# Kernel tuning notes

Measured on AMD Instinct MI355X. Metric: run time of the kernel, lower is better.

Reference implementation:

```python
import jax, jax.numpy as jnp
import numpy as np

HEADS = 4
OUT_CH = 32
NEG_SLOPE = 0.2  # PyG GATConv default leaky_relu slope


def setup_inputs() -> dict:
    key = jax.random.key(0)
    ks = jax.random.split(key, 8)
    N, E, C_IN = 500000, 1500000, 128
    x = jax.random.normal(ks[0], (N, C_IN), dtype=jnp.float32)
    edge_index = jax.random.randint(ks[1], (2, E), 0, N, dtype=jnp.int64)
    # GATConv params (lin weight, attention vectors, bias)
    W = jax.random.normal(ks[2], (C_IN, HEADS * OUT_CH), dtype=jnp.float32) * (1.0 / np.sqrt(C_IN))
    att_src = jax.random.normal(ks[3], (HEADS, OUT_CH), dtype=jnp.float32) * 0.1
    att_dst = jax.random.normal(ks[4], (HEADS, OUT_CH), dtype=jnp.float32) * 0.1
    bias = jnp.zeros((HEADS * OUT_CH,), dtype=jnp.float32)
    # fc head
    fc_w = jax.random.normal(ks[5], (HEADS * OUT_CH, 1), dtype=jnp.float32) * (1.0 / np.sqrt(HEADS * OUT_CH))
    fc_b = jnp.zeros((1,), dtype=jnp.float32)
    return {"x": x, "edge_index": edge_index, "W": W, "att_src": att_src,
            "att_dst": att_dst, "bias": bias, "fc_w": fc_w, "fc_b": fc_b}


def reference(x, edge_index, W, att_src, att_dst, bias, fc_w, fc_b):
    N = x.shape[0]
    # PyG GATConv adds self-loops by default
    loops = jnp.arange(N, dtype=edge_index.dtype)
    src = jnp.concatenate([edge_index[0], loops])  # [Etot]
    dst = jnp.concatenate([edge_index[1], loops])  # [Etot]

    h = (x @ W).reshape(N, HEADS, OUT_CH)                # [N,H,C]
    a_src = jnp.einsum('nhc,hc->nh', h, att_src)          # [N,H]
    a_dst = jnp.einsum('nhc,hc->nh', h, att_dst)          # [N,H]

    e = a_src[src] + a_dst[dst]                           # [Etot,H]
    e = jax.nn.leaky_relu(e, NEG_SLOPE)
    # segment softmax over incoming edges of each dst node
    e_max = jax.ops.segment_max(e, dst, num_segments=N)   # [N,H]
    e_exp = jnp.exp(e - e_max[dst])
    e_sum = jax.ops.segment_sum(e_exp, dst, num_segments=N)
    alpha = e_exp / e_sum[dst]                            # [Etot,H]

    msg = h[src] * alpha[:, :, None]                      # [Etot,H,C]
    out = jax.ops.segment_sum(msg, dst, num_segments=N)   # [N,H,C]
    out = out.reshape(N, HEADS * OUT_CH) + bias

    out = jax.nn.relu(out)
    logits = out @ fc_w + fc_b                            # [N,1]
    return jax.nn.sigmoid(logits)
```

## Files before the change

kernel.cpp:

```cpp
#include <hip/hip_runtime.h>

typedef __attribute__((ext_vector_type(8))) short bf16x8;
typedef __attribute__((ext_vector_type(4))) float f32x4;

__device__ __forceinline__ unsigned short f2bf(float f){
  unsigned int u = __builtin_bit_cast(unsigned int, f);
  u += 0x7fffu + ((u >> 16) & 1u);
  return (unsigned short)(u >> 16);
}
__device__ __forceinline__ float bf_lo(unsigned int v){
  return __builtin_bit_cast(float, v << 16);
}
__device__ __forceinline__ float bf_hi(unsigned int v){
  return __builtin_bit_cast(float, v & 0xffff0000u);
}
__device__ __forceinline__ float lrelu(float x){ return x > 0.f ? x : 0.2f * x; }

#define GLOAD_LDS16(g, l) \
  __builtin_amdgcn_global_load_lds((const __attribute__((address_space(1))) unsigned int*)(g), \
                                   (__attribute__((address_space(3))) unsigned int*)(l), 16, 0, 0)

__global__ __launch_bounds__(256) void k_init(const float* __restrict__ W,
                                              unsigned short* __restrict__ WbfT,
                                              int4* __restrict__ deg4, int n4){
  int i = blockIdx.x * 256 + threadIdx.x;
  if (i < n4){ int4 z; z.x=0; z.y=0; z.z=0; z.w=0; deg4[i] = z; }
  if (i < 128*128){
    int c = i & 127, k = i >> 7;
    WbfT[c * 136 + k] = f2bf(W[k * 128 + c]);
  }
}

__global__ __launch_bounds__(256) void k_gemm(
    const float* __restrict__ x, const unsigned short* __restrict__ WbfT,
    const float* __restrict__ attS, const float* __restrict__ attD,
    unsigned short* __restrict__ h, float* __restrict__ aS, float* __restrict__ aD,
    int N, int nslices)
{
  __shared__ unsigned short Wt[128][136];
  __shared__ float xbuf[4][3][16*128];
  int tid = threadIdx.x;

  const char* wsrc = (const char*)WbfT;
  #pragma unroll
  for (int it = 0; it < 9; ++it){
    int i = it * 256 + tid;
    if (i < 2176) GLOAD_LDS16(wsrc + (size_t)i * 16, ((char*)Wt) + i * 16);
  }
  __syncthreads();

  int wv = tid >> 6, lane = tid & 63;
  int lrow = lane & 15, lgrp = lane >> 4;

  int slice  = (int)blockIdx.x * 4 + wv;
  int stride = (int)gridDim.x * 4;

  auto STAGE = [&](int s, int b){
    if (s >= nslices) s = nslices - 1;
    char* dst0 = (char*)&xbuf[wv][b][0];
    #pragma unroll
    for (int k = 0; k < 8; ++k){
      int c = k * 64 + lane;
      int r = c >> 5, j = c & 31;
      int gr = s * 16 + r; if (gr >= N) gr = N - 1;
      const char* src = (const char*)(x + (size_t)gr * 128) + ((j ^ (r & 7)) << 4);
      GLOAD_LDS16(src, dst0 + k * 1024);
    }
  };

  STAGE(slice, 0);
  STAGE(slice + stride, 1);
  int bi = 0;

  for (int s = slice; s < nslices; s += stride){
    STAGE(s + 2 * stride, (bi + 2) % 3);
    asm volatile("s_waitcnt vmcnt(16)" ::: "memory");

    const f32x4* xb = (const f32x4*)&xbuf[wv][bi][0];
    bf16x8 af[4];
    #pragma unroll
    for (int kt = 0; kt < 4; ++kt){
      int j0 = kt * 8 + lgrp * 2;
      f32x4 lo = xb[lrow * 32 + ( j0      ^ (lrow & 7))];
      f32x4 hi = xb[lrow * 32 + ((j0 + 1) ^ (lrow & 7))];
      bf16x8 a;
      #pragma unroll
      for (int j = 0; j < 4; ++j){
        a[j]   = (short)f2bf(lo[j]);
        a[4+j] = (short)f2bf(hi[j]);
      }
      af[kt] = a;
    }

    f32x4 acc[8];
    #pragma unroll
    for (int ct = 0; ct < 8; ++ct){ acc[ct][0]=0.f; acc[ct][1]=0.f; acc[ct][2]=0.f; acc[ct][3]=0.f; }
    #pragma unroll
    for (int kt = 0; kt < 4; ++kt){
      #pragma unroll
      for (int ct = 0; ct < 8; ++ct){
        bf16x8 bw = *(const bf16x8*)&Wt[ct*16 + lrow][kt*32 + lgrp*8];
        acc[ct] = __builtin_amdgcn_mfma_f32_16x16x32_bf16(bw, af[kt], acc[ct], 0, 0, 0);
      }
    }

    int row = s * 16 + lrow;
    float ps[4] = {0.f,0.f,0.f,0.f}, pd[4] = {0.f,0.f,0.f,0.f};
    #pragma unroll
    for (int ct = 0; ct < 8; ++ct){
      int hh = ct >> 1;
      f32x4 s4 = *(const f32x4*)(attS + ct*16 + lgrp*4);
      f32x4 d4 = *(const f32x4*)(attD + ct*16 + lgrp*4);
      #pragma unroll
      for (int g = 0; g < 4; ++g){
        ps[hh] += acc[ct][g] * s4[g];
        pd[hh] += acc[ct][g] * d4[g];
      }
    }
    #pragma unroll
    for (int hh = 0; hh < 4; ++hh){
      ps[hh] += __shfl_xor(ps[hh], 16, 64);
      ps[hh] += __shfl_xor(ps[hh], 32, 64);
      pd[hh] += __shfl_xor(pd[hh], 16, 64);
      pd[hh] += __shfl_xor(pd[hh], 32, 64);
    }
    if (lgrp == 0 && row < N){
      f32x4 vs, vd;
      #pragma unroll
      for (int hh = 0; hh < 4; ++hh){ vs[hh] = ps[hh]; vd[hh] = pd[hh]; }
      *(f32x4*)(aS + (size_t)row * 4) = vs;
      *(f32x4*)(aD + (size_t)row * 4) = vd;
    }
    if (row < N){
      unsigned short* hp = h + (size_t)row * 128 + lgrp * 4;
      #pragma unroll
      for (int ct = 0; ct < 8; ++ct){
        unsigned int u0 = (unsigned int)f2bf(acc[ct][0])
                        | ((unsigned int)f2bf(acc[ct][1]) << 16);
        unsigned int u1 = (unsigned int)f2bf(acc[ct][2])
                        | ((unsigned int)f2bf(acc[ct][3]) << 16);
        uint2 u; u.x = u0; u.y = u1;
        *(uint2*)(hp + ct * 16) = u;
      }
    }
    bi = (bi + 1) % 3;
  }
}

__global__ __launch_bounds__(256) void k_hist(const int* __restrict__ dst, int E,
                                              int* __restrict__ deg){
  int e = blockIdx.x * 256 + threadIdx.x;
  if (e < E) atomicAdd(&deg[dst[e]], 1);
}

__global__ __launch_bounds__(256) void k_chunksum(const int* __restrict__ deg, int N,
                                                  int* __restrict__ bsum){
  __shared__ int sm[256];
  int tid = threadIdx.x;
  int base = blockIdx.x * 2048 + tid * 8;
  int s = 0;
  #pragma unroll
  for (int j = 0; j < 8; ++j) s += (base + j < N) ? deg[base + j] : 0;
  sm[tid] = s; __syncthreads();
  for (int off = 128; off > 0; off >>= 1){
    if (tid < off) sm[tid] += sm[tid + off];
    __syncthreads();
  }
  if (tid == 0) bsum[blockIdx.x] = sm[0];
}

__global__ __launch_bounds__(256) void k_scansums(int* __restrict__ bsum, int nb){
  __shared__ int sm[256];
  int tid = threadIdx.x;
  int carry = 0;
  for (int base = 0; base < nb; base += 256){
    int v = (base + tid < nb) ? bsum[base + tid] : 0;
    sm[tid] = v; __syncthreads();
    for (int off = 1; off < 256; off <<= 1){
      int t = (tid >= off) ? sm[tid - off] : 0;
      __syncthreads();
      sm[tid] += t;
      __syncthreads();
    }
    int incl = sm[tid];
    int total = sm[255];
    __syncthreads();
    if (base + tid < nb) bsum[base + tid] = carry + incl - v;
    carry += total;
  }
}

__global__ __launch_bounds__(256) void k_scanfinal(const int* __restrict__ deg,
    const int* __restrict__ bsum, int N, int E,
    int* __restrict__ rowptr, int* __restrict__ cursor){
  __shared__ int sm[256];
  int tid = threadIdx.x;
  int base = blockIdx.x * 2048 + tid * 8;
  int v[8];
  #pragma unroll
  for (int j = 0; j < 8; ++j) v[j] = (base + j < N) ? deg[base + j] : 0;
  int t = 0;
  #pragma unroll
  for (int j = 0; j < 8; ++j){ int x_ = v[j]; v[j] = t; t += x_; }
  sm[tid] = t; __syncthreads();
  for (int off = 1; off < 256; off <<= 1){
    int u = (tid >= off) ? sm[tid - off] : 0;
    __syncthreads();
    sm[tid] += u;
    __syncthreads();
  }
  int excl = sm[tid] - t;
  int off0 = bsum[blockIdx.x] + excl;
  #pragma unroll
  for (int j = 0; j < 8; ++j){
    if (base + j < N){
      int val = off0 + v[j];
      rowptr[base + j] = val;
      cursor[base + j] = val;
    }
  }
  if (blockIdx.x == 0 && tid == 0) rowptr[N] = E;
}

__global__ __launch_bounds__(256) void k_scatter(const int* __restrict__ src,
    const int* __restrict__ dst, int E, int* __restrict__ cursor,
    const float* __restrict__ aS, const float* __restrict__ aD,
    int* __restrict__ csr, float* __restrict__ wexp){
  int e = blockIdx.x * 256 + threadIdx.x;
  if (e < E){
    int s = src[e], d = dst[e];
    int p = atomicAdd(&cursor[d], 1);
    csr[p] = s;
    f32x4 as = *(const f32x4*)(aS + (size_t)s * 4);
    f32x4 ad = *(const f32x4*)(aD + (size_t)d * 4);
    f32x4 w;
    #pragma unroll
    for (int hh = 0; hh < 4; ++hh) w[hh] = __expf(lrelu(as[hh] + ad[hh]));
    *(f32x4*)(wexp + (size_t)p * 4) = w;
  }
}

__global__ __launch_bounds__(256) void k_aggr(
    const uint4* __restrict__ h4, const float* __restrict__ aS,
    const float* __restrict__ aD, const int* __restrict__ rowptr,
    const int* __restrict__ csr, const float* __restrict__ wexp,
    const float* __restrict__ bias, const float* __restrict__ fcw,
    const float* __restrict__ fcb, float* __restrict__ out, int N)
{
  int lane = threadIdx.x & 63;
  int l16  = lane & 15;
  int node = ((int)blockIdx.x * 256 + (int)threadIdx.x) >> 4;
  if (node >= N) return;
  int head = l16 >> 2;

  float wself = __expf(lrelu(aS[node * 4 + head] + aD[node * 4 + head]));
  float wsum  = wself;

  float acc[8];
  {
    uint4 hv = h4[node * 16 + l16];
    acc[0] = wself * bf_lo(hv.x);  acc[1] = wself * bf_hi(hv.x);
    acc[2] = wself * bf_lo(hv.y);  acc[3] = wself * bf_hi(hv.y);
    acc[4] = wself * bf_lo(hv.z);  acc[5] = wself * bf_hi(hv.z);
    acc[6] = wself * bf_lo(hv.w);  acc[7] = wself * bf_hi(hv.w);
  }

  int rb = rowptr[node], re = rowptr[node + 1];
  for (int j = rb; j < re; j += 4){
    int i1 = (j + 1 < re) ? j + 1 : j;
    int i2 = (j + 2 < re) ? j + 2 : j;
    int i3 = (j + 3 < re) ? j + 3 : j;
    int s0 = csr[j], s1 = csr[i1], s2 = csr[i2], s3 = csr[i3];
    float m1 = (j + 1 < re) ? 1.f : 0.f;
    float m2 = (j + 2 < re) ? 1.f : 0.f;
    float m3 = (j + 3 < re) ? 1.f : 0.f;
    float w0 = wexp[(size_t)j  * 4 + head];
    float w1 = wexp[(size_t)i1 * 4 + head] * m1;
    float w2 = wexp[(size_t)i2 * 4 + head] * m2;
    float w3 = wexp[(size_t)i3 * 4 + head] * m3;
    uint4 v0 = h4[(size_t)s0 * 16 + l16];
    uint4 v1 = h4[(size_t)s1 * 16 + l16];
    uint4 v2 = h4[(size_t)s2 * 16 + l16];
    uint4 v3 = h4[(size_t)s3 * 16 + l16];
    wsum += w0 + w1 + w2 + w3;
    acc[0] += w0*bf_lo(v0.x) + w1*bf_lo(v1.x) + w2*bf_lo(v2.x) + w3*bf_lo(v3.x);
    acc[1] += w0*bf_hi(v0.x) + w1*bf_hi(v1.x) + w2*bf_hi(v2.x) + w3*bf_hi(v3.x);
    acc[2] += w0*bf_lo(v0.y) + w1*bf_lo(v1.y) + w2*bf_lo(v2.y) + w3*bf_lo(v3.y);
    acc[3] += w0*bf_hi(v0.y) + w1*bf_hi(v1.y) + w2*bf_hi(v2.y) + w3*bf_hi(v3.y);
    acc[4] += w0*bf_lo(v0.z) + w1*bf_lo(v1.z) + w2*bf_lo(v2.z) + w3*bf_lo(v3.z);
    acc[5] += w0*bf_hi(v0.z) + w1*bf_hi(v1.z) + w2*bf_hi(v2.z) + w3*bf_hi(v3.z);
    acc[6] += w0*bf_lo(v0.w) + w1*bf_lo(v1.w) + w2*bf_lo(v2.w) + w3*bf_lo(v3.w);
    acc[7] += w0*bf_hi(v0.w) + w1*bf_hi(v1.w) + w2*bf_hi(v2.w) + w3*bf_hi(v3.w);
  }

  float inv = 1.f / wsum;
  const float* bp = bias + l16 * 8;
  const float* fp = fcw  + l16 * 8;
  f32x4 b0 = *(const f32x4*)bp,      b1 = *(const f32x4*)(bp + 4);
  f32x4 f0 = *(const f32x4*)fp,      f1 = *(const f32x4*)(fp + 4);
  float p = 0.f;
  p += fmaxf(acc[0]*inv + b0[0], 0.f) * f0[0];
  p += fmaxf(acc[1]*inv + b0[1], 0.f) * f0[1];
  p += fmaxf(acc[2]*inv + b0[2], 0.f) * f0[2];
  p += fmaxf(acc[3]*inv + b0[3], 0.f) * f0[3];
  p += fmaxf(acc[4]*inv + b1[0], 0.f) * f1[0];
  p += fmaxf(acc[5]*inv + b1[1], 0.f) * f1[1];
  p += fmaxf(acc[6]*inv + b1[2], 0.f) * f1[2];
  p += fmaxf(acc[7]*inv + b1[3], 0.f) * f1[3];
  #pragma unroll
  for (int m = 1; m < 16; m <<= 1) p += __shfl_xor(p, m, 64);
  if (l16 == 0) out[node] = 1.f / (1.f + __expf(-(p + fcb[0])));
}

extern "C" void kernel_launch(void* const* d_in, const int* in_sizes, int n_in,
                              void* d_out, int out_size, void* d_ws, size_t ws_size,
                              hipStream_t stream) {
  const float* x    = (const float*)d_in[0];
  const int*   ei   = (const int*)  d_in[1];
  const float* W    = (const float*)d_in[2];
  const float* attS = (const float*)d_in[3];
  const float* attD = (const float*)d_in[4];
  const float* bias = (const float*)d_in[5];
  const float* fcw  = (const float*)d_in[6];
  const float* fcb  = (const float*)d_in[7];

  int N = in_sizes[0] / 128;
  int E = in_sizes[1] / 2;
  const int* srcA = ei;
  const int* dstA = ei + E;

  char* ws = (char*)d_ws;
  size_t off = 0;
  auto alloc = [&](size_t bytes) -> void* {
    void* p = ws + off;
    off += (bytes + 255) & ~(size_t)255;
    return p;
  };
  unsigned short* h  = (unsigned short*)alloc((size_t)N * 128 * 2);
  float* aS   = (float*)alloc((size_t)N * 4 * 4);
  float* aD   = (float*)alloc((size_t)N * 4 * 4);
  int* deg    = (int*)alloc((size_t)N * 4);
  int* rowptr = (int*)alloc(((size_t)N + 1) * 4);
  int* cursor = (int*)alloc((size_t)N * 4);
  int* csr    = (int*)alloc((size_t)E * 4);
  float* wexp = (float*)alloc((size_t)E * 4 * 4);
  int* bsum   = (int*)alloc(4096);
  unsigned short* WbfT = (unsigned short*)alloc(128 * 136 * 2);

  int n4 = (N + 3) / 4;
  int ninit = (n4 > 16384) ? n4 : 16384;
  k_init<<<(ninit + 255) / 256, 256, 0, stream>>>(W, WbfT, (int4*)deg, n4);
  int nslices = (N + 15) / 16;
  k_gemm<<<256, 256, 0, stream>>>(x, WbfT, attS, attD, h, aS, aD, N, nslices);
  k_hist<<<(E + 255) / 256, 256, 0, stream>>>(dstA, E, deg);
  int nb = (N + 2047) / 2048;
  k_chunksum<<<nb, 256, 0, stream>>>(deg, N, bsum);
  k_scansums<<<1, 256, 0, stream>>>(bsum, nb);
  k_scanfinal<<<nb, 256, 0, stream>>>(deg, bsum, N, E, rowptr, cursor);
  k_scatter<<<(E + 255) / 256, 256, 0, stream>>>(srcA, dstA, E, cursor, aS, aD,
                                                 csr, wexp);
  k_aggr<<<(N + 15) / 16, 256, 0, stream>>>((const uint4*)h, aS, aD, rowptr, csr,
                                            wexp, bias, fcw, fcb, (float*)d_out, N);
}
```

Baseline: 366.6 us.

## Stage x through registers with bf16 LDS tile and double-buffered loads in GEMM

Replaces the async global-to-LDS triple-buffered fp32 staging of x in the projection GEMM with register double-buffering. Each wave converts its loaded rows to bf16 once and writes them to a compact bf16 LDS tile before the MFMA operand loads. Launch size grows to 512 blocks of 512 threads (8 waves per block) to raise occupancy and memory parallelism. The change halves LDS footprint per slice and removes per-lane redundant conversions. In exchange it holds 16 float4 loads in VGPRs and relies on the compiler to overlap the loads with compute.

```diff
diff --git a/kernel.cpp b/kernel.cpp
--- a/kernel.cpp
+++ b/kernel.cpp
@@ -7,6 +7,9 @@
   unsigned int u = __builtin_bit_cast(unsigned int, f);
   u += 0x7fffu + ((u >> 16) & 1u);
   return (unsigned short)(u >> 16);
+}
+__device__ __forceinline__ unsigned int pack2(float a, float b){
+  return (unsigned int)f2bf(a) | ((unsigned int)f2bf(b) << 16);
 }
 __device__ __forceinline__ float bf_lo(unsigned int v){
   return __builtin_bit_cast(float, v << 16);
@@ -31,66 +34,55 @@
   }
 }
 
-__global__ __launch_bounds__(256) void k_gemm(
+__global__ __launch_bounds__(512) void k_gemm(
     const float* __restrict__ x, const unsigned short* __restrict__ WbfT,
     const float* __restrict__ attS, const float* __restrict__ attD,
     unsigned short* __restrict__ h, float* __restrict__ aS, float* __restrict__ aD,
     int N, int nslices)
 {
   __shared__ unsigned short Wt[128][136];
-  __shared__ float xbuf[4][3][16*128];
+  __shared__ unsigned short xt[8][16][136];
   int tid = threadIdx.x;
 
   const char* wsrc = (const char*)WbfT;
   #pragma unroll
-  for (int it = 0; it < 9; ++it){
-    int i = it * 256 + tid;
+  for (int it = 0; it < 5; ++it){
+    int i = it * 512 + tid;
     if (i < 2176) GLOAD_LDS16(wsrc + (size_t)i * 16, ((char*)Wt) + i * 16);
   }
   __syncthreads();
 
   int wv = tid >> 6, lane = tid & 63;
   int lrow = lane & 15, lgrp = lane >> 4;
-
-  int slice  = (int)blockIdx.x * 4 + wv;
-  int stride = (int)gridDim.x * 4;
-
-  auto STAGE = [&](int s, int b){
+  int r2 = lane >> 5;
+  int j  = lane & 31;
+
+  int slice0 = (int)blockIdx.x * 8 + wv;
+  int stride = (int)gridDim.x * 8;
+
+  auto LOADS = [&](f32x4* v, int s){
     if (s >= nslices) s = nslices - 1;
-    char* dst0 = (char*)&xbuf[wv][b][0];
     #pragma unroll
     for (int k = 0; k < 8; ++k){
-      int c = k * 64 + lane;
-      int r = c >> 5, j = c & 31;
-      int gr = s * 16 + r; if (gr >= N) gr = N - 1;
-      const char* src = (const char*)(x + (size_t)gr * 128) + ((j ^ (r & 7)) << 4);
-      GLOAD_LDS16(src, dst0 + k * 1024);
+      int gr = s * 16 + k * 2 + r2;
+      if (gr >= N) gr = N - 1;
+      v[k] = *(const f32x4*)(x + (size_t)gr * 128 + j * 4);
     }
   };
 
-  STAGE(slice, 0);
-  STAGE(slice + stride, 1);
-  int bi = 0;
-
-  for (int s = slice; s < nslices; s += stride){
-    STAGE(s + 2 * stride, (bi + 2) % 3);
-    asm volatile("s_waitcnt vmcnt(16)" ::: "memory");
-
-    const f32x4* xb = (const f32x4*)&xbuf[wv][bi][0];
+  auto COMP = [&](f32x4* v, int s){
+    if (s >= nslices) return;
+    #pragma unroll
+    for (int k = 0; k < 8; ++k){
+      uint2 u;
+      u.x = pack2(v[k][0], v[k][1]);
+      u.y = pack2(v[k][2], v[k][3]);
+      *(uint2*)&xt[wv][k*2 + r2][j*4] = u;
+    }
     bf16x8 af[4];
     #pragma unroll
-    for (int kt = 0; kt < 4; ++kt){
-      int j0 = kt * 8 + lgrp * 2;
-      f32x4 lo = xb[lrow * 32 + ( j0      ^ (lrow & 7))];
-      f32x4 hi = xb[lrow * 32 + ((j0 + 1) ^ (lrow & 7))];
-      bf16x8 a;
-      #pragma unroll
-      for (int j = 0; j < 4; ++j){
-        a[j]   = (short)f2bf(lo[j]);
-        a[4+j] = (short)f2bf(hi[j]);
-      }
-      af[kt] = a;
-    }
+    for (int kt = 0; kt < 4; ++kt)
+      af[kt] = *(const bf16x8*)&xt[wv][lrow][kt*32 + lgrp*8];
 
     f32x4 acc[8];
     #pragma unroll
@@ -143,7 +135,15 @@
         *(uint2*)(hp + ct * 16) = u;
       }
     }
-    bi = (bi + 1) % 3;
+  };
+
+  f32x4 vA[8], vB[8];
+  LOADS(vA, slice0);
+  for (int s = slice0; s < nslices; s += 2 * stride){
+    LOADS(vB, s + stride);
+    COMP(vA, s);
+    LOADS(vA, s + 2 * stride);
+    COMP(vB, s + stride);
   }
 }
 
@@ -351,7 +351,7 @@
   int ninit = (n4 > 16384) ? n4 : 16384;
   k_init<<<(ninit + 255) / 256, 256, 0, stream>>>(W, WbfT, (int4*)deg, n4);
   int nslices = (N + 15) / 16;
-  k_gemm<<<256, 256, 0, stream>>>(x, WbfT, attS, attD, h, aS, aD, N, nslices);
+  k_gemm<<<512, 512, 0, stream>>>(x, WbfT, attS, attD, h, aS, aD, N, nslices);
   k_hist<<<(E + 255) / 256, 256, 0, stream>>>(dstA, E, deg);
   int nb = (N + 2047) / 2048;
   k_chunksum<<<nb, 256, 0, stream>>>(deg, N, bsum);
```

Result: slower. 436.5 us (+19.1%).

## Store edge weights head-planar and use aligned vector loads in aggregation

Applied to the files above, without the earlier changes.

Edge weights are now stored as four per-head planes instead of interleaved [E,4], and the aggregation loop starts at a 4-aligned index so it can fetch four CSR indices and four weights with one 16-byte load each, masking entries outside the node's row. This is meant to cut the number of scalar gather loads in the hot aggregation loop. In exchange, the scatter kernel does four strided scalar stores instead of one vector store, and the padded csr tail is zeroed so out-of-range lanes gather node 0 harmlessly.

```diff
diff --git a/kernel.cpp b/kernel.cpp
--- a/kernel.cpp
+++ b/kernel.cpp
@@ -22,9 +22,11 @@
 
 __global__ __launch_bounds__(256) void k_init(const float* __restrict__ W,
                                               unsigned short* __restrict__ WbfT,
-                                              int4* __restrict__ deg4, int n4){
+                                              int4* __restrict__ deg4, int n4,
+                                              int* __restrict__ csr, int E){
   int i = blockIdx.x * 256 + threadIdx.x;
   if (i < n4){ int4 z; z.x=0; z.y=0; z.z=0; z.w=0; deg4[i] = z; }
+  if (i < 4) csr[E + i] = 0;
   if (i < 128*128){
     int c = i & 127, k = i >> 7;
     WbfT[c * 136 + k] = f2bf(W[k * 128 + c]);
@@ -223,9 +225,9 @@
 }
 
 __global__ __launch_bounds__(256) void k_scatter(const int* __restrict__ src,
-    const int* __restrict__ dst, int E, int* __restrict__ cursor,
+    const int* __restrict__ dst, int E, int Epad, int* __restrict__ cursor,
     const float* __restrict__ aS, const float* __restrict__ aD,
-    int* __restrict__ csr, float* __restrict__ wexp){
+    int* __restrict__ csr, float* __restrict__ wexpt){
   int e = blockIdx.x * 256 + threadIdx.x;
   if (e < E){
     int s = src[e], d = dst[e];
@@ -233,25 +235,25 @@
     csr[p] = s;
     f32x4 as = *(const f32x4*)(aS + (size_t)s * 4);
     f32x4 ad = *(const f32x4*)(aD + (size_t)d * 4);
-    f32x4 w;
-    #pragma unroll
-    for (int hh = 0; hh < 4; ++hh) w[hh] = __expf(lrelu(as[hh] + ad[hh]));
-    *(f32x4*)(wexp + (size_t)p * 4) = w;
+    #pragma unroll
+    for (int hh = 0; hh < 4; ++hh)
+      wexpt[(size_t)hh * Epad + p] = __expf(lrelu(as[hh] + ad[hh]));
   }
 }
 
 __global__ __launch_bounds__(256) void k_aggr(
     const uint4* __restrict__ h4, const float* __restrict__ aS,
     const float* __restrict__ aD, const int* __restrict__ rowptr,
-    const int* __restrict__ csr, const float* __restrict__ wexp,
+    const int* __restrict__ csr, const float* __restrict__ wexpt,
     const float* __restrict__ bias, const float* __restrict__ fcw,
-    const float* __restrict__ fcb, float* __restrict__ out, int N)
+    const float* __restrict__ fcb, float* __restrict__ out, int N, int Epad)
 {
   int lane = threadIdx.x & 63;
   int l16  = lane & 15;
   int node = ((int)blockIdx.x * 256 + (int)threadIdx.x) >> 4;
   if (node >= N) return;
   int head = l16 >> 2;
+  const float* wplane = wexpt + (size_t)head * Epad;
 
   float wself = __expf(lrelu(aS[node * 4 + head] + aD[node * 4 + head]));
   float wsum  = wself;
@@ -266,22 +268,17 @@
   }
 
   int rb = rowptr[node], re = rowptr[node + 1];
-  for (int j = rb; j < re; j += 4){
-    int i1 = (j + 1 < re) ? j + 1 : j;
-    int i2 = (j + 2 < re) ? j + 2 : j;
-    int i3 = (j + 3 < re) ? j + 3 : j;
-    int s0 = csr[j], s1 = csr[i1], s2 = csr[i2], s3 = csr[i3];
-    float m1 = (j + 1 < re) ? 1.f : 0.f;
-    float m2 = (j + 2 < re) ? 1.f : 0.f;
-    float m3 = (j + 3 < re) ? 1.f : 0.f;
-    float w0 = wexp[(size_t)j  * 4 + head];
-    float w1 = wexp[(size_t)i1 * 4 + head] * m1;
-    float w2 = wexp[(size_t)i2 * 4 + head] * m2;
-    float w3 = wexp[(size_t)i3 * 4 + head] * m3;
-    uint4 v0 = h4[(size_t)s0 * 16 + l16];
-    uint4 v1 = h4[(size_t)s1 * 16 + l16];
-    uint4 v2 = h4[(size_t)s2 * 16 + l16];
-    uint4 v3 = h4[(size_t)s3 * 16 + l16];
+  for (int j = rb & ~3; j < re; j += 4){
+    int4  s4 = *(const int4*)(csr + j);
+    f32x4 w4 = *(const f32x4*)(wplane + j);
+    float w0 = (j     >= rb && j     < re) ? w4[0] : 0.f;
+    float w1 = (j + 1 >= rb && j + 1 < re) ? w4[1] : 0.f;
+    float w2 = (j + 2 >= rb && j + 2 < re) ? w4[2] : 0.f;
+    float w3 = (j + 3 >= rb && j + 3 < re) ? w4[3] : 0.f;
+    uint4 v0 = h4[(size_t)s4.x * 16 + l16];
+    uint4 v1 = h4[(size_t)s4.y * 16 + l16];
+    uint4 v2 = h4[(size_t)s4.z * 16 + l16];
+    uint4 v3 = h4[(size_t)s4.w * 16 + l16];
     wsum += w0 + w1 + w2 + w3;
     acc[0] += w0*bf_lo(v0.x) + w1*bf_lo(v1.x) + w2*bf_lo(v2.x) + w3*bf_lo(v3.x);
     acc[1] += w0*bf_hi(v0.x) + w1*bf_hi(v1.x) + w2*bf_hi(v2.x) + w3*bf_hi(v3.x);
@@ -326,6 +323,7 @@
 
   int N = in_sizes[0] / 128;
   int E = in_sizes[1] / 2;
+  int Epad = ((E + 3) & ~3) + 4;
   const int* srcA = ei;
   const int* dstA = ei + E;
 
@@ -342,14 +340,14 @@
   int* deg    = (int*)alloc((size_t)N * 4);
   int* rowptr = (int*)alloc(((size_t)N + 1) * 4);
   int* cursor = (int*)alloc((size_t)N * 4);
-  int* csr    = (int*)alloc((size_t)E * 4);
-  float* wexp = (float*)alloc((size_t)E * 4 * 4);
+  int* csr    = (int*)alloc((size_t)Epad * 4);
+  float* wexpt= (float*)alloc((size_t)Epad * 4 * 4);
   int* bsum   = (int*)alloc(4096);
   unsigned short* WbfT = (unsigned short*)alloc(128 * 136 * 2);
 
   int n4 = (N + 3) / 4;
   int ninit = (n4 > 16384) ? n4 : 16384;
-  k_init<<<(ninit + 255) / 256, 256, 0, stream>>>(W, WbfT, (int4*)deg, n4);
+  k_init<<<(ninit + 255) / 256, 256, 0, stream>>>(W, WbfT, (int4*)deg, n4, csr, E);
   int nslices = (N + 15) / 16;
   k_gemm<<<256, 256, 0, stream>>>(x, WbfT, attS, attD, h, aS, aD, N, nslices);
   k_hist<<<(E + 255) / 256, 256, 0, stream>>>(dstA, E, deg);
@@ -357,8 +355,9 @@
   k_chunksum<<<nb, 256, 0, stream>>>(deg, N, bsum);
   k_scansums<<<1, 256, 0, stream>>>(bsum, nb);
   k_scanfinal<<<nb, 256, 0, stream>>>(deg, bsum, N, E, rowptr, cursor);
-  k_scatter<<<(E + 255) / 256, 256, 0, stream>>>(srcA, dstA, E, cursor, aS, aD,
-                                                 csr, wexp);
+  k_scatter<<<(E + 255) / 256, 256, 0, stream>>>(srcA, dstA, E, Epad, cursor,
+                                                 aS, aD, csr, wexpt);
   k_aggr<<<(N + 15) / 16, 256, 0, stream>>>((const uint4*)h, aS, aD, rowptr, csr,
-                                            wexp, bias, fcw, fcb, (float*)d_out, N);
-}
+                                            wexpt, bias, fcw, fcb, (float*)d_out,
+                                            N, Epad);
+}
```

New measurement: 437.3 us. +19.3%, slower.
